# Kernel tuning notes

Measured on AMD Instinct MI355X. Metric: run time of the kernel, lower is better.

Reference implementation:

```python
import jax, jax.numpy as jnp
import numpy as np

B, D = 16384, 512


def setup_inputs() -> dict:
    key = jax.random.key(0)
    ks = jax.random.split(key, 7)
    s1 = 1.0 / np.sqrt(D + 1)
    s2 = 1.0 / np.sqrt(2 * D + 1)
    return {
        "t": jax.random.uniform(ks[0], (1,), dtype=jnp.float32),
        "z": jax.random.normal(ks[1], (B, D), dtype=jnp.float32),
        "logp_z": jnp.zeros((B, 1), dtype=jnp.float32),
        "W1": jax.random.normal(ks[2], (2 * D, D + 1), dtype=jnp.float32) * s1,
        "b1": jax.random.normal(ks[3], (2 * D,), dtype=jnp.float32) * s1,
        "W2": jax.random.normal(ks[4], (D, 2 * D + 1), dtype=jnp.float32) * s2,
        "b2": jax.random.normal(ks[5], (D,), dtype=jnp.float32) * s2,
    }


def reference(t, z, logp_z, W1, b1, W2, b2):
    # CNF dynamics: dz/dt = fc2(concat(relu(fc1(concat(z, t))), t))
    batch = z.shape[0]
    tt = jnp.full((batch, 1), t[0], dtype=z.dtype)
    x = jnp.concatenate([z, tt], axis=1)            # [B, D+1]
    h_pre = x @ W1.T + b1                           # [B, 2D]
    h = jax.nn.relu(h_pre)
    x2 = jnp.concatenate([h, tt], axis=1)           # [B, 2D+1]
    dz_dt = x2 @ W2.T + b2                          # [B, D]

    # Exact Jacobian trace of linear-relu-linear block (closed form of the
    # per-dim autograd loop in trace_df_dz):
    #   tr J = sum_h relu'(h_pre[:,h]) * (sum_i W2[i,h] * W1[h,i])
    W2h = W2[:, : 2 * D]                            # drop time column, [D, 2D]
    W1z = W1[:, :D]                                 # drop time column, [2D, D]
    c = jnp.sum(W2h.T * W1z, axis=1)                # [2D]
    mask = (h_pre > 0).astype(z.dtype)              # relu'
    trace = mask @ c                                # [B]
    dlogp_z_dt = -trace[:, None]                    # [B, 1]
    return dz_dt, dlogp_z_dt
```

## Files before the change

### kernel.cpp

```cpp
#include <hip/hip_runtime.h>
#include <stdint.h>

#define B_   16384
#define D_   512
#define N1_  1024
#define K1_  512
#define N2_  512
#define K2_  1024

#define DELTA     4e-3f
#define RCAP      16u
#define OCAP      64u

typedef _Float16 f16x8 __attribute__((ext_vector_type(8)));
typedef _Float16 f16x4 __attribute__((ext_vector_type(4)));
typedef float    f32x4 __attribute__((ext_vector_type(4)));

#define MFMA(a, b, c) __builtin_amdgcn_mfma_f32_16x16x32_f16(a, b, c, 0, 0, 0)

__global__ __launch_bounds__(256) void prep_w(
    const float* __restrict__ t,
    const float* __restrict__ W1, const float* __restrict__ b1,
    const float* __restrict__ W2, const float* __restrict__ b2,
    _Float16* __restrict__ wp,
    float* __restrict__ bias1, float* __restrict__ bias2,
    float* __restrict__ cvec) {
  int blk = blockIdx.x, tid = threadIdx.x;
  if (blk < 512) {
    int idx = blk * 256 + tid;
    int g = idx >> 11, rem = idx & 2047;
    int w = rem >> 8, nt = (rem >> 6) & 3, lane = rem & 63;
    int m16 = lane & 15, q = lane >> 4;
    int ch = g >> 5, ph = g & 31;
    const float* src;
    float scale;
    if (ph < 16) {
      int col = ch * 512 + w * 64 + nt * 16 + m16;
      int k = ph * 32 + q * 8;
      src = W1 + (size_t)col * 513 + k;
      scale = 64.f;
    } else {
      int col = w * 64 + nt * 16 + m16;
      int k = ch * 512 + (ph - 16) * 32 + q * 8;
      src = W2 + (size_t)col * 1025 + k;
      scale = 1.f;
    }
    f16x8 hv;
    #pragma unroll
    for (int e = 0; e < 8; ++e) hv[e] = (_Float16)(src[e] * scale);
    *(f16x8*)(wp + (size_t)idx * 8) = hv;
  } else if (blk < 516) {
    int j = (blk - 512) * 256 + tid;
    float t0 = t[0];
    bias1[j] = b1[j] + t0 * W1[(size_t)j * 513 + 512];
    if (j < 512) bias2[j] = b2[j] + t0 * W2[(size_t)j * 1025 + 1024];
  } else {
    int wave = tid >> 6, lane = tid & 63;
    int j = (blk - 516) * 4 + wave;
    float s = 0.f;
    #pragma unroll
    for (int kk = 0; kk < 8; ++kk) {
      int k = lane + kk * 64;
      s += W2[(size_t)k * 1025 + j] * W1[(size_t)j * 513 + k];
    }
    #pragma unroll
    for (int off = 32; off > 0; off >>= 1) s += __shfl_xor(s, off);
    if (lane == 0) cvec[j] = s;
  }
}


__global__ __launch_bounds__(512) void fused_kernel(
    const float* __restrict__ z, const _Float16* __restrict__ wp,
    const float* __restrict__ W1f,
    const float* __restrict__ bias1, const float* __restrict__ bias2,
    const float* __restrict__ cvec,
    float* __restrict__ out, float* __restrict__ dlogp) {
  __shared__ __align__(16) _Float16 Az[64 * 512];
  __shared__ __align__(16) _Float16 Hb[64 * 512];
  __shared__ __align__(16) float bias1L[1024];
  __shared__ __align__(16) float cvecL[1024];
  __shared__ uint32_t rbuck[64][RCAP];
  __shared__ uint32_t rbcnt[64];
  __shared__ uint32_t ovf[OCAP];
  __shared__ float redbuf[8][64];
  __shared__ float fixv[64];
  __shared__ float fixo[64];
  __shared__ uint32_t ovfcnt;

  const int tid  = threadIdx.x;
  const int lane = tid & 63, w = tid >> 6;
  const int q    = lane >> 4, m16 = lane & 15;
  const int sw   = m16 & 7;
  const int bm   = blockIdx.x;

  if (tid < 64) { rbcnt[tid] = 0; fixo[tid] = 0.f; }
  if (tid == 0) ovfcnt = 0;

  {
    const float* zp = z + (size_t)bm * 64 * 512;
    #pragma unroll
    for (int i = 0; i < 16; ++i) {
      int slot = i * 512 + tid;
      int row = slot >> 7, u8 = slot & 127;
      f32x4 v = *(const f32x4*)(zp + (size_t)row * 512 + u8 * 4);
      f16x4 hv;
      #pragma unroll
      for (int r = 0; r < 4; ++r) hv[r] = (_Float16)(v[r] * 16.f);
      int gz = (u8 >> 1) ^ (row & 7);
      *(f16x4*)((char*)Az + row * 1024 + gz * 16 + (u8 & 1) * 8) = hv;
    }
  }
  for (int i = tid; i < 1024; i += 512) {
    bias1L[i] = bias1[i];
    cvecL[i]  = cvec[i];
  }
  __syncthreads();

  f32x4 acc1[4][4] = {};
  f32x4 acc2[4][4] = {};
  float tr[4] = {0.f, 0.f, 0.f, 0.f};

  const char* azb   = (const char*)Az + m16 * 1024;
  const char* hbb   = (const char*)Hb + m16 * 1024;
  const char* wbase = (const char*)wp + w * 4096 + lane * 16;

  f16x8 cwA[4], cwB[4];
  #pragma unroll
  for (int nt = 0; nt < 4; ++nt) cwA[nt] = *(const f16x8*)(wbase + nt * 1024);

  for (int ch = 0; ch < 2; ++ch) {
    for (int s2 = 0; s2 < 8; ++s2) {
      const int s = s2 * 2;
      const int g = ch * 32 + s;
      #pragma unroll
      for (int nt = 0; nt < 4; ++nt)
        cwB[nt] = *(const f16x8*)(wbase + (size_t)(g + 1) * 32768 + nt * 1024);
      {
        const int zg = ((s * 4 + q) ^ sw) << 4;
        f16x8 zf0 = *(const f16x8*)(azb + 0 * 16384 + zg);
        f16x8 zf1 = *(const f16x8*)(azb + 1 * 16384 + zg);
        f16x8 zf2 = *(const f16x8*)(azb + 2 * 16384 + zg);
        f16x8 zf3 = *(const f16x8*)(azb + 3 * 16384 + zg);
        __builtin_amdgcn_s_setprio(1);
        #pragma unroll
        for (int nt = 0; nt < 4; ++nt) {
          acc1[0][nt] = MFMA(cwA[nt], zf0, acc1[0][nt]);
          acc1[1][nt] = MFMA(cwA[nt], zf1, acc1[1][nt]);
          acc1[2][nt] = MFMA(cwA[nt], zf2, acc1[2][nt]);
          acc1[3][nt] = MFMA(cwA[nt], zf3, acc1[3][nt]);
        }
        __builtin_amdgcn_s_setprio(0);
      }
      {
        const int gn = (g + 2 > 63) ? 63 : (g + 2);
        #pragma unroll
        for (int nt = 0; nt < 4; ++nt)
          cwA[nt] = *(const f16x8*)(wbase + (size_t)gn * 32768 + nt * 1024);
      }
      {
        const int zg = (((s + 1) * 4 + q) ^ sw) << 4;
        f16x8 zf0 = *(const f16x8*)(azb + 0 * 16384 + zg);
        f16x8 zf1 = *(const f16x8*)(azb + 1 * 16384 + zg);
        f16x8 zf2 = *(const f16x8*)(azb + 2 * 16384 + zg);
        f16x8 zf3 = *(const f16x8*)(azb + 3 * 16384 + zg);
        __builtin_amdgcn_s_setprio(1);
        #pragma unroll
        for (int nt = 0; nt < 4; ++nt) {
          acc1[0][nt] = MFMA(cwB[nt], zf0, acc1[0][nt]);
          acc1[1][nt] = MFMA(cwB[nt], zf1, acc1[1][nt]);
          acc1[2][nt] = MFMA(cwB[nt], zf2, acc1[2][nt]);
          acc1[3][nt] = MFMA(cwB[nt], zf3, acc1[3][nt]);
        }
        __builtin_amdgcn_s_setprio(0);
      }
    }

    __syncthreads();

    #pragma unroll
    for (int nt = 0; nt < 4; ++nt) {
      int colc = w * 64 + nt * 16 + q * 4;
      int col = ch * 512 + colc;
      f32x4 b4 = *(const f32x4*)&bias1L[col];
      f32x4 c4 = *(const f32x4*)&cvecL[col];
      #pragma unroll
      for (int mt = 0; mt < 4; ++mt) {
        int row = mt * 16 + m16;
        f16x4 hv;
        #pragma unroll
        for (int r = 0; r < 4; ++r) {
          float hp = acc1[mt][nt][r] * (1.f / 1024.f) + b4[r];
          hv[r] = (_Float16)(hp > 0.f ? hp : 0.f);
          if (hp > 0.f) tr[mt] += c4[r];
          if (__builtin_fabsf(hp) < DELTA) {
            uint32_t e = (uint32_t)(col + r) | (hp > 0.f ? 0x80000000u : 0u);
            uint32_t bi = atomicAdd(&rbcnt[row], 1u);
            if (bi < RCAP) rbuck[row][bi] = e;
            else {
              uint32_t oi = atomicAdd(&ovfcnt, 1u);
              if (oi < OCAP) ovf[oi] = ((uint32_t)row << 10) | e;
            }
          }
        }
        int gg = (colc >> 3) ^ (row & 7);
        *(f16x4*)((char*)Hb + row * 1024 + gg * 16 + (q & 1) * 8) = hv;
        acc1[mt][nt] = (f32x4){0.f, 0.f, 0.f, 0.f};
      }
    }

    __syncthreads();

    for (int t2 = 0; t2 < 8; ++t2) {
      const int t = t2 * 2;
      const int g = ch * 32 + 16 + t;
      #pragma unroll
      for (int nt = 0; nt < 4; ++nt)
        cwB[nt] = *(const f16x8*)(wbase + (size_t)(g + 1) * 32768 + nt * 1024);
      {
        const int hg = ((t * 4 + q) ^ sw) << 4;
        f16x8 hf0 = *(const f16x8*)(hbb + 0 * 16384 + hg);
        f16x8 hf1 = *(const f16x8*)(hbb + 1 * 16384 + hg);
        f16x8 hf2 = *(const f16x8*)(hbb + 2 * 16384 + hg);
        f16x8 hf3 = *(const f16x8*)(hbb + 3 * 16384 + hg);
        __builtin_amdgcn_s_setprio(1);
        #pragma unroll
        for (int nt = 0; nt < 4; ++nt) {
          acc2[0][nt] = MFMA(cwA[nt], hf0, acc2[0][nt]);
          acc2[1][nt] = MFMA(cwA[nt], hf1, acc2[1][nt]);
          acc2[2][nt] = MFMA(cwA[nt], hf2, acc2[2][nt]);
          acc2[3][nt] = MFMA(cwA[nt], hf3, acc2[3][nt]);
        }
        __builtin_amdgcn_s_setprio(0);
      }
      {
        const int gn = (g + 2 > 63) ? 63 : (g + 2);
        #pragma unroll
        for (int nt = 0; nt < 4; ++nt)
          cwA[nt] = *(const f16x8*)(wbase + (size_t)gn * 32768 + nt * 1024);
      }
      {
        const int hg = (((t + 1) * 4 + q) ^ sw) << 4;
        f16x8 hf0 = *(const f16x8*)(hbb + 0 * 16384 + hg);
        f16x8 hf1 = *(const f16x8*)(hbb + 1 * 16384 + hg);
        f16x8 hf2 = *(const f16x8*)(hbb + 2 * 16384 + hg);
        f16x8 hf3 = *(const f16x8*)(hbb + 3 * 16384 + hg);
        __builtin_amdgcn_s_setprio(1);
        #pragma unroll
        for (int nt = 0; nt < 4; ++nt) {
          acc2[0][nt] = MFMA(cwB[nt], hf0, acc2[0][nt]);
          acc2[1][nt] = MFMA(cwB[nt], hf1, acc2[1][nt]);
          acc2[2][nt] = MFMA(cwB[nt], hf2, acc2[2][nt]);
          acc2[3][nt] = MFMA(cwB[nt], hf3, acc2[3][nt]);
        }
        __builtin_amdgcn_s_setprio(0);
      }
    }
  }

  #pragma unroll
  for (int mt = 0; mt < 4; ++mt) {
    int row = bm * 64 + mt * 16 + m16;
    #pragma unroll
    for (int nt = 0; nt < 4; ++nt) {
      int col = w * 64 + nt * 16 + q * 4;
      f32x4 b2v = *(const f32x4*)(bias2 + col);
      *(f32x4*)(out + (size_t)row * 512 + col) = acc2[mt][nt] + b2v;
    }
  }

  #pragma unroll
  for (int mt = 0; mt < 4; ++mt) {
    tr[mt] += __shfl_xor(tr[mt], 16);
    tr[mt] += __shfl_xor(tr[mt], 32);
  }
  if (q == 0) {
    #pragma unroll
    for (int mt = 0; mt < 4; ++mt) redbuf[w][mt * 16 + m16] = tr[mt];
  }
  __syncthreads();

  #pragma unroll 1
  for (int r8 = 0; r8 < 8; ++r8) {
    int row = w * 8 + r8;
    uint32_t cnt = rbcnt[row];
    if (cnt > RCAP) cnt = RCAP;
    float corr = 0.f;
    if (cnt) {
      const float* zr = z + ((size_t)(bm * 64 + row)) * 512;
      float zv[8];
      #pragma unroll
      for (int it = 0; it < 8; ++it) zv[it] = zr[it * 64 + lane];
      for (uint32_t e = 0; e < cnt; ++e) {
        uint32_t en = rbuck[row][e];
        int col  = (int)(en & 1023u);
        int oldm = (int)(en >> 31);
        const float* wc = W1f + (size_t)col * 513;
        float s = 0.f;
        #pragma unroll
        for (int it = 0; it < 8; ++it) s += zv[it] * wc[it * 64 + lane];
        #pragma unroll
        for (int off = 32; off > 0; off >>= 1) s += __shfl_xor(s, off);
        float hp = s + bias1L[col];
        int newm = hp > 0.f ? 1 : 0;
        if (newm != oldm) corr += oldm ? cvecL[col] : -cvecL[col];
      }
    }
    if (lane == 0) fixv[row] = corr;
  }
  {
    uint32_t on = ovfcnt;
    if (on > OCAP) on = OCAP;
    for (uint32_t i = w; i < on; i += 8) {
      uint32_t e = ovf[i];
      int row  = (int)((e >> 10) & 63u);
      int col  = (int)(e & 1023u);
      int oldm = (int)(e >> 31);
      const float* zr = z + ((size_t)(bm * 64 + row)) * 512;
      const float* wc = W1f + (size_t)col * 513;
      float s = 0.f;
      #pragma unroll
      for (int it = 0; it < 8; ++it) {
        int k = it * 64 + lane;
        s += zr[k] * wc[k];
      }
      #pragma unroll
      for (int off = 32; off > 0; off >>= 1) s += __shfl_xor(s, off);
      if (lane == 0) {
        float hp = s + bias1L[col];
        int newm = hp > 0.f ? 1 : 0;
        if (newm != oldm) atomicAdd(&fixo[row], oldm ? cvecL[col] : -cvecL[col]);
      }
    }
  }
  __syncthreads();

  if (tid < 64) {
    float s = 0.f;
    #pragma unroll
    for (int ww = 0; ww < 8; ++ww) s += redbuf[ww][tid];
    dlogp[bm * 64 + tid] = -s + fixv[tid] + fixo[tid];
  }
}

extern "C" void kernel_launch(void* const* d_in, const int* in_sizes, int n_in,
                              void* d_out, int out_size, void* d_ws, size_t ws_size,
                              hipStream_t stream) {
  const float* t  = (const float*)d_in[0];
  const float* z  = (const float*)d_in[1];
  const float* W1 = (const float*)d_in[3];
  const float* b1 = (const float*)d_in[4];
  const float* W2 = (const float*)d_in[5];
  const float* b2 = (const float*)d_in[6];

  float* out   = (float*)d_out;
  float* dlogp = out + (size_t)B_ * D_;

  char* ws = (char*)d_ws;
  _Float16* wp    = (_Float16*)ws; ws += (size_t)64 * 32768;
  float*    bias1 = (float*)ws;    ws += 1024 * 4;
  float*    bias2 = (float*)ws;    ws += 512 * 4;
  float*    cvec  = (float*)ws;    ws += 1024 * 4;

  prep_w<<<772, 256, 0, stream>>>(t, W1, b1, W2, b2, wp, bias1, bias2, cvec);
  fused_kernel<<<256, 512, 0, stream>>>(z, wp, W1, bias1, bias2, cvec, out, dlogp);
}
```

Baseline: 157.5 us.

## Halve row tile to 32 and drop weight double-buffering for higher occupancy

Each block now processes 32 rows instead of 64, doubling the grid to 512 blocks and halving the shared-memory and accumulator footprint. The explicit register double-buffering of weight fragments is replaced with a simpler unrolled loop, and launch bounds request more resident waves. This targets latency hiding through occupancy, but weights are reloaded twice as often per row, so L2 traffic roughly doubles. The tighter register bound may also cause spills.

```diff
diff --git a/kernel.cpp b/kernel.cpp
--- a/kernel.cpp
+++ b/kernel.cpp
@@ -10,7 +10,7 @@
 
 #define DELTA     4e-3f
 #define RCAP      16u
-#define OCAP      64u
+#define OCAP      32u
 
 typedef _Float16 f16x8 __attribute__((ext_vector_type(8)));
 typedef _Float16 f16x4 __attribute__((ext_vector_type(4)));
@@ -70,22 +70,22 @@
 }
 
 
-__global__ __launch_bounds__(512) void fused_kernel(
+__global__ __launch_bounds__(512, 4) void fused_kernel(
     const float* __restrict__ z, const _Float16* __restrict__ wp,
     const float* __restrict__ W1f,
     const float* __restrict__ bias1, const float* __restrict__ bias2,
     const float* __restrict__ cvec,
     float* __restrict__ out, float* __restrict__ dlogp) {
-  __shared__ __align__(16) _Float16 Az[64 * 512];
-  __shared__ __align__(16) _Float16 Hb[64 * 512];
+  __shared__ __align__(16) _Float16 Az[32 * 512];
+  __shared__ __align__(16) _Float16 Hb[32 * 512];
   __shared__ __align__(16) float bias1L[1024];
   __shared__ __align__(16) float cvecL[1024];
-  __shared__ uint32_t rbuck[64][RCAP];
-  __shared__ uint32_t rbcnt[64];
+  __shared__ uint32_t rbuck[32][RCAP];
+  __shared__ uint32_t rbcnt[32];
   __shared__ uint32_t ovf[OCAP];
-  __shared__ float redbuf[8][64];
-  __shared__ float fixv[64];
-  __shared__ float fixo[64];
+  __shared__ float redbuf[8][32];
+  __shared__ float fixv[32];
+  __shared__ float fixo[32];
   __shared__ uint32_t ovfcnt;
 
   const int tid  = threadIdx.x;
@@ -94,13 +94,13 @@
   const int sw   = m16 & 7;
   const int bm   = blockIdx.x;
 
-  if (tid < 64) { rbcnt[tid] = 0; fixo[tid] = 0.f; }
+  if (tid < 32) { rbcnt[tid] = 0; fixo[tid] = 0.f; }
   if (tid == 0) ovfcnt = 0;
 
   {
-    const float* zp = z + (size_t)bm * 64 * 512;
-    #pragma unroll
-    for (int i = 0; i < 16; ++i) {
+    const float* zp = z + (size_t)bm * 32 * 512;
+    #pragma unroll
+    for (int i = 0; i < 8; ++i) {
       int slot = i * 512 + tid;
       int row = slot >> 7, u8 = slot & 127;
       f32x4 v = *(const f32x4*)(zp + (size_t)row * 512 + u8 * 4);
@@ -117,63 +117,35 @@
   }
   __syncthreads();
 
-  f32x4 acc1[4][4] = {};
-  f32x4 acc2[4][4] = {};
-  float tr[4] = {0.f, 0.f, 0.f, 0.f};
+  f32x4 acc1[2][4] = {};
+  f32x4 acc2[2][4] = {};
+  float tr[2] = {0.f, 0.f};
 
   const char* azb   = (const char*)Az + m16 * 1024;
   const char* hbb   = (const char*)Hb + m16 * 1024;
   const char* wbase = (const char*)wp + w * 4096 + lane * 16;
 
-  f16x8 cwA[4], cwB[4];
-  #pragma unroll
-  for (int nt = 0; nt < 4; ++nt) cwA[nt] = *(const f16x8*)(wbase + nt * 1024);
-
   for (int ch = 0; ch < 2; ++ch) {
-    for (int s2 = 0; s2 < 8; ++s2) {
-      const int s = s2 * 2;
-      const int g = ch * 32 + s;
-      #pragma unroll
-      for (int nt = 0; nt < 4; ++nt)
-        cwB[nt] = *(const f16x8*)(wbase + (size_t)(g + 1) * 32768 + nt * 1024);
-      {
-        const int zg = ((s * 4 + q) ^ sw) << 4;
-        f16x8 zf0 = *(const f16x8*)(azb + 0 * 16384 + zg);
-        f16x8 zf1 = *(const f16x8*)(azb + 1 * 16384 + zg);
-        f16x8 zf2 = *(const f16x8*)(azb + 2 * 16384 + zg);
-        f16x8 zf3 = *(const f16x8*)(azb + 3 * 16384 + zg);
-        __builtin_amdgcn_s_setprio(1);
-        #pragma unroll
-        for (int nt = 0; nt < 4; ++nt) {
-          acc1[0][nt] = MFMA(cwA[nt], zf0, acc1[0][nt]);
-          acc1[1][nt] = MFMA(cwA[nt], zf1, acc1[1][nt]);
-          acc1[2][nt] = MFMA(cwA[nt], zf2, acc1[2][nt]);
-          acc1[3][nt] = MFMA(cwA[nt], zf3, acc1[3][nt]);
-        }
-        __builtin_amdgcn_s_setprio(0);
-      }
-      {
-        const int gn = (g + 2 > 63) ? 63 : (g + 2);
-        #pragma unroll
-        for (int nt = 0; nt < 4; ++nt)
-          cwA[nt] = *(const f16x8*)(wbase + (size_t)gn * 32768 + nt * 1024);
-      }
-      {
-        const int zg = (((s + 1) * 4 + q) ^ sw) << 4;
-        f16x8 zf0 = *(const f16x8*)(azb + 0 * 16384 + zg);
-        f16x8 zf1 = *(const f16x8*)(azb + 1 * 16384 + zg);
-        f16x8 zf2 = *(const f16x8*)(azb + 2 * 16384 + zg);
-        f16x8 zf3 = *(const f16x8*)(azb + 3 * 16384 + zg);
-        __builtin_amdgcn_s_setprio(1);
-        #pragma unroll
-        for (int nt = 0; nt < 4; ++nt) {
-          acc1[0][nt] = MFMA(cwB[nt], zf0, acc1[0][nt]);
-          acc1[1][nt] = MFMA(cwB[nt], zf1, acc1[1][nt]);
-          acc1[2][nt] = MFMA(cwB[nt], zf2, acc1[2][nt]);
-          acc1[3][nt] = MFMA(cwB[nt], zf3, acc1[3][nt]);
-        }
-        __builtin_amdgcn_s_setprio(0);
-      }
+    #pragma unroll 4
+    for (int s = 0; s < 16; ++s) {
+      const char* wsl = wbase + (size_t)(ch * 32 + s) * 32768;
+      f16x8 cw0 = *(const f16x8*)(wsl);
+      f16x8 cw1 = *(const f16x8*)(wsl + 1024);
+      f16x8 cw2 = *(const f16x8*)(wsl + 2048);
+      f16x8 cw3 = *(const f16x8*)(wsl + 3072);
+      const int zg = ((s * 4 + q) ^ sw) << 4;
+      f16x8 zf0 = *(const f16x8*)(azb + zg);
+      f16x8 zf1 = *(const f16x8*)(azb + 16384 + zg);
+      __builtin_amdgcn_s_setprio(1);
+      acc1[0][0] = MFMA(cw0, zf0, acc1[0][0]);
+      acc1[0][1] = MFMA(cw1, zf0, acc1[0][1]);
+      acc1[0][2] = MFMA(cw2, zf0, acc1[0][2]);
+      acc1[0][3] = MFMA(cw3, zf0, acc1[0][3]);
+      acc1[1][0] = MFMA(cw0, zf1, acc1[1][0]);
+      acc1[1][1] = MFMA(cw1, zf1, acc1[1][1]);
+      acc1[1][2] = MFMA(cw2, zf1, acc1[1][2]);
+      acc1[1][3] = MFMA(cw3, zf1, acc1[1][3]);
+      __builtin_amdgcn_s_setprio(0);
     }
 
     __syncthreads();
@@ -185,7 +157,7 @@
       f32x4 b4 = *(const f32x4*)&bias1L[col];
       f32x4 c4 = *(const f32x4*)&cvecL[col];
       #pragma unroll
-      for (int mt = 0; mt < 4; ++mt) {
+      for (int mt = 0; mt < 2; ++mt) {
         int row = mt * 16 + m16;
         f16x4 hv;
         #pragma unroll
@@ -211,56 +183,32 @@
 
     __syncthreads();
 
-    for (int t2 = 0; t2 < 8; ++t2) {
-      const int t = t2 * 2;
-      const int g = ch * 32 + 16 + t;
-      #pragma unroll
-      for (int nt = 0; nt < 4; ++nt)
-        cwB[nt] = *(const f16x8*)(wbase + (size_t)(g + 1) * 32768 + nt * 1024);
-      {
-        const int hg = ((t * 4 + q) ^ sw) << 4;
-        f16x8 hf0 = *(const f16x8*)(hbb + 0 * 16384 + hg);
-        f16x8 hf1 = *(const f16x8*)(hbb + 1 * 16384 + hg);
-        f16x8 hf2 = *(const f16x8*)(hbb + 2 * 16384 + hg);
-        f16x8 hf3 = *(const f16x8*)(hbb + 3 * 16384 + hg);
-        __builtin_amdgcn_s_setprio(1);
-        #pragma unroll
-        for (int nt = 0; nt < 4; ++nt) {
-          acc2[0][nt] = MFMA(cwA[nt], hf0, acc2[0][nt]);
-          acc2[1][nt] = MFMA(cwA[nt], hf1, acc2[1][nt]);
-          acc2[2][nt] = MFMA(cwA[nt], hf2, acc2[2][nt]);
-          acc2[3][nt] = MFMA(cwA[nt], hf3, acc2[3][nt]);
-        }
-        __builtin_amdgcn_s_setprio(0);
-      }
-      {
-        const int gn = (g + 2 > 63) ? 63 : (g + 2);
-        #pragma unroll
-        for (int nt = 0; nt < 4; ++nt)
-          cwA[nt] = *(const f16x8*)(wbase + (size_t)gn * 32768 + nt * 1024);
-      }
-      {
-        const int hg = (((t + 1) * 4 + q) ^ sw) << 4;
-        f16x8 hf0 = *(const f16x8*)(hbb + 0 * 16384 + hg);
-        f16x8 hf1 = *(const f16x8*)(hbb + 1 * 16384 + hg);
-        f16x8 hf2 = *(const f16x8*)(hbb + 2 * 16384 + hg);
-        f16x8 hf3 = *(const f16x8*)(hbb + 3 * 16384 + hg);
-        __builtin_amdgcn_s_setprio(1);
-        #pragma unroll
-        for (int nt = 0; nt < 4; ++nt) {
-          acc2[0][nt] = MFMA(cwB[nt], hf0, acc2[0][nt]);
-          acc2[1][nt] = MFMA(cwB[nt], hf1, acc2[1][nt]);
-          acc2[2][nt] = MFMA(cwB[nt], hf2, acc2[2][nt]);
-          acc2[3][nt] = MFMA(cwB[nt], hf3, acc2[3][nt]);
-        }
-        __builtin_amdgcn_s_setprio(0);
-      }
+    #pragma unroll 4
+    for (int t = 0; t < 16; ++t) {
+      const char* wsl = wbase + (size_t)(ch * 32 + 16 + t) * 32768;
+      f16x8 cw0 = *(const f16x8*)(wsl);
+      f16x8 cw1 = *(const f16x8*)(wsl + 1024);
+      f16x8 cw2 = *(const f16x8*)(wsl + 2048);
+      f16x8 cw3 = *(const f16x8*)(wsl + 3072);
+      const int hg = ((t * 4 + q) ^ sw) << 4;
+      f16x8 hf0 = *(const f16x8*)(hbb + hg);
+      f16x8 hf1 = *(const f16x8*)(hbb + 16384 + hg);
+      __builtin_amdgcn_s_setprio(1);
+      acc2[0][0] = MFMA(cw0, hf0, acc2[0][0]);
+      acc2[0][1] = MFMA(cw1, hf0, acc2[0][1]);
+      acc2[0][2] = MFMA(cw2, hf0, acc2[0][2]);
+      acc2[0][3] = MFMA(cw3, hf0, acc2[0][3]);
+      acc2[1][0] = MFMA(cw0, hf1, acc2[1][0]);
+      acc2[1][1] = MFMA(cw1, hf1, acc2[1][1]);
+      acc2[1][2] = MFMA(cw2, hf1, acc2[1][2]);
+      acc2[1][3] = MFMA(cw3, hf1, acc2[1][3]);
+      __builtin_amdgcn_s_setprio(0);
     }
   }
 
   #pragma unroll
-  for (int mt = 0; mt < 4; ++mt) {
-    int row = bm * 64 + mt * 16 + m16;
+  for (int mt = 0; mt < 2; ++mt) {
+    int row = bm * 32 + mt * 16 + m16;
     #pragma unroll
     for (int nt = 0; nt < 4; ++nt) {
       int col = w * 64 + nt * 16 + q * 4;
@@ -270,24 +218,24 @@
   }
 
   #pragma unroll
-  for (int mt = 0; mt < 4; ++mt) {
+  for (int mt = 0; mt < 2; ++mt) {
     tr[mt] += __shfl_xor(tr[mt], 16);
     tr[mt] += __shfl_xor(tr[mt], 32);
   }
   if (q == 0) {
     #pragma unroll
-    for (int mt = 0; mt < 4; ++mt) redbuf[w][mt * 16 + m16] = tr[mt];
+    for (int mt = 0; mt < 2; ++mt) redbuf[w][mt * 16 + m16] = tr[mt];
   }
   __syncthreads();
 
   #pragma unroll 1
-  for (int r8 = 0; r8 < 8; ++r8) {
-    int row = w * 8 + r8;
+  for (int r4 = 0; r4 < 4; ++r4) {
+    int row = w * 4 + r4;
     uint32_t cnt = rbcnt[row];
     if (cnt > RCAP) cnt = RCAP;
     float corr = 0.f;
     if (cnt) {
-      const float* zr = z + ((size_t)(bm * 64 + row)) * 512;
+      const float* zr = z + ((size_t)(bm * 32 + row)) * 512;
       float zv[8];
       #pragma unroll
       for (int it = 0; it < 8; ++it) zv[it] = zr[it * 64 + lane];
@@ -313,10 +261,10 @@
     if (on > OCAP) on = OCAP;
     for (uint32_t i = w; i < on; i += 8) {
       uint32_t e = ovf[i];
-      int row  = (int)((e >> 10) & 63u);
+      int row  = (int)((e >> 10) & 31u);
       int col  = (int)(e & 1023u);
       int oldm = (int)(e >> 31);
-      const float* zr = z + ((size_t)(bm * 64 + row)) * 512;
+      const float* zr = z + ((size_t)(bm * 32 + row)) * 512;
       const float* wc = W1f + (size_t)col * 513;
       float s = 0.f;
       #pragma unroll
@@ -335,11 +283,11 @@
   }
   __syncthreads();
 
-  if (tid < 64) {
+  if (tid < 32) {
     float s = 0.f;
     #pragma unroll
     for (int ww = 0; ww < 8; ++ww) s += redbuf[ww][tid];
-    dlogp[bm * 64 + tid] = -s + fixv[tid] + fixo[tid];
+    dlogp[bm * 32 + tid] = -s + fixv[tid] + fixo[tid];
   }
 }
 
@@ -363,5 +311,5 @@
   float*    cvec  = (float*)ws;    ws += 1024 * 4;
 
   prep_w<<<772, 256, 0, stream>>>(t, W1, b1, W2, b2, wp, bias1, bias2, cvec);
-  fused_kernel<<<256, 512, 0, stream>>>(z, wp, W1, bias1, bias2, cvec, out, dlogp);
+  fused_kernel<<<512, 512, 0, stream>>>(z, wp, W1, bias1, bias2, cvec, out, dlogp);
 }
```

Result: slower. 162.9 us (+3.4%).

## Double waves per block to 16 with half-width N tiles and prefetch W1 rows in fixup

Applied to the files above, without the earlier changes.

Raises the fused kernel block from 512 to 1024 threads. Each of the 16 waves now owns 32 output columns instead of 64, which halves per-wave accumulator and weight-register state and doubles the waves available to hide MFMA and load latency. The near-threshold fixup loop also prefetches the next W1 row while reducing the current one, and the overflow capacity is reduced. The cost is that each loaded z/h fragment feeds fewer MFMAs, LDS fragment traffic per FLOP rises, and register pressure is constrained by the 1024-thread launch bound.

```diff
diff --git a/kernel.cpp b/kernel.cpp
--- a/kernel.cpp
+++ b/kernel.cpp
@@ -10,7 +10,7 @@
 
 #define DELTA     4e-3f
 #define RCAP      16u
-#define OCAP      64u
+#define OCAP      32u
 
 typedef _Float16 f16x8 __attribute__((ext_vector_type(8)));
 typedef _Float16 f16x4 __attribute__((ext_vector_type(4)));
@@ -70,7 +70,7 @@
 }
 
 
-__global__ __launch_bounds__(512) void fused_kernel(
+__global__ __launch_bounds__(1024, 4) void fused_kernel(
     const float* __restrict__ z, const _Float16* __restrict__ wp,
     const float* __restrict__ W1f,
     const float* __restrict__ bias1, const float* __restrict__ bias2,
@@ -83,7 +83,7 @@
   __shared__ uint32_t rbuck[64][RCAP];
   __shared__ uint32_t rbcnt[64];
   __shared__ uint32_t ovf[OCAP];
-  __shared__ float redbuf[8][64];
+  __shared__ float redbuf[16][64];
   __shared__ float fixv[64];
   __shared__ float fixo[64];
   __shared__ uint32_t ovfcnt;
@@ -100,8 +100,8 @@
   {
     const float* zp = z + (size_t)bm * 64 * 512;
     #pragma unroll
-    for (int i = 0; i < 16; ++i) {
-      int slot = i * 512 + tid;
+    for (int i = 0; i < 8; ++i) {
+      int slot = i * 1024 + tid;
       int row = slot >> 7, u8 = slot & 127;
       f32x4 v = *(const f32x4*)(zp + (size_t)row * 512 + u8 * 4);
       f16x4 hv;
@@ -111,67 +111,67 @@
       *(f16x4*)((char*)Az + row * 1024 + gz * 16 + (u8 & 1) * 8) = hv;
     }
   }
-  for (int i = tid; i < 1024; i += 512) {
-    bias1L[i] = bias1[i];
-    cvecL[i]  = cvec[i];
+  if (tid < 1024) {
+    bias1L[tid] = bias1[tid];
+    cvecL[tid]  = cvec[tid];
   }
   __syncthreads();
 
-  f32x4 acc1[4][4] = {};
-  f32x4 acc2[4][4] = {};
+  f32x4 acc1[4][2] = {};
+  f32x4 acc2[4][2] = {};
   float tr[4] = {0.f, 0.f, 0.f, 0.f};
 
   const char* azb   = (const char*)Az + m16 * 1024;
   const char* hbb   = (const char*)Hb + m16 * 1024;
-  const char* wbase = (const char*)wp + w * 4096 + lane * 16;
-
-  f16x8 cwA[4], cwB[4];
-  #pragma unroll
-  for (int nt = 0; nt < 4; ++nt) cwA[nt] = *(const f16x8*)(wbase + nt * 1024);
+  const char* wbase = (const char*)wp + (w >> 1) * 4096 + (w & 1) * 2048 + lane * 16;
+
+  f16x8 cwA[2], cwB[2];
+  cwA[0] = *(const f16x8*)(wbase);
+  cwA[1] = *(const f16x8*)(wbase + 1024);
 
   for (int ch = 0; ch < 2; ++ch) {
     for (int s2 = 0; s2 < 8; ++s2) {
       const int s = s2 * 2;
       const int g = ch * 32 + s;
-      #pragma unroll
-      for (int nt = 0; nt < 4; ++nt)
-        cwB[nt] = *(const f16x8*)(wbase + (size_t)(g + 1) * 32768 + nt * 1024);
+      cwB[0] = *(const f16x8*)(wbase + (size_t)(g + 1) * 32768);
+      cwB[1] = *(const f16x8*)(wbase + (size_t)(g + 1) * 32768 + 1024);
       {
         const int zg = ((s * 4 + q) ^ sw) << 4;
-        f16x8 zf0 = *(const f16x8*)(azb + 0 * 16384 + zg);
-        f16x8 zf1 = *(const f16x8*)(azb + 1 * 16384 + zg);
-        f16x8 zf2 = *(const f16x8*)(azb + 2 * 16384 + zg);
-        f16x8 zf3 = *(const f16x8*)(azb + 3 * 16384 + zg);
+        f16x8 zf0 = *(const f16x8*)(azb + zg);
+        f16x8 zf1 = *(const f16x8*)(azb + 16384 + zg);
+        f16x8 zf2 = *(const f16x8*)(azb + 32768 + zg);
+        f16x8 zf3 = *(const f16x8*)(azb + 49152 + zg);
         __builtin_amdgcn_s_setprio(1);
-        #pragma unroll
-        for (int nt = 0; nt < 4; ++nt) {
-          acc1[0][nt] = MFMA(cwA[nt], zf0, acc1[0][nt]);
-          acc1[1][nt] = MFMA(cwA[nt], zf1, acc1[1][nt]);
-          acc1[2][nt] = MFMA(cwA[nt], zf2, acc1[2][nt]);
-          acc1[3][nt] = MFMA(cwA[nt], zf3, acc1[3][nt]);
-        }
+        acc1[0][0] = MFMA(cwA[0], zf0, acc1[0][0]);
+        acc1[0][1] = MFMA(cwA[1], zf0, acc1[0][1]);
+        acc1[1][0] = MFMA(cwA[0], zf1, acc1[1][0]);
+        acc1[1][1] = MFMA(cwA[1], zf1, acc1[1][1]);
+        acc1[2][0] = MFMA(cwA[0], zf2, acc1[2][0]);
+        acc1[2][1] = MFMA(cwA[1], zf2, acc1[2][1]);
+        acc1[3][0] = MFMA(cwA[0], zf3, acc1[3][0]);
+        acc1[3][1] = MFMA(cwA[1], zf3, acc1[3][1]);
         __builtin_amdgcn_s_setprio(0);
       }
       {
         const int gn = (g + 2 > 63) ? 63 : (g + 2);
-        #pragma unroll
-        for (int nt = 0; nt < 4; ++nt)
-          cwA[nt] = *(const f16x8*)(wbase + (size_t)gn * 32768 + nt * 1024);
+        cwA[0] = *(const f16x8*)(wbase + (size_t)gn * 32768);
+        cwA[1] = *(const f16x8*)(wbase + (size_t)gn * 32768 + 1024);
       }
       {
         const int zg = (((s + 1) * 4 + q) ^ sw) << 4;
-        f16x8 zf0 = *(const f16x8*)(azb + 0 * 16384 + zg);
-        f16x8 zf1 = *(const f16x8*)(azb + 1 * 16384 + zg);
-        f16x8 zf2 = *(const f16x8*)(azb + 2 * 16384 + zg);
-        f16x8 zf3 = *(const f16x8*)(azb + 3 * 16384 + zg);
+        f16x8 zf0 = *(const f16x8*)(azb + zg);
+        f16x8 zf1 = *(const f16x8*)(azb + 16384 + zg);
+        f16x8 zf2 = *(const f16x8*)(azb + 32768 + zg);
+        f16x8 zf3 = *(const f16x8*)(azb + 49152 + zg);
         __builtin_amdgcn_s_setprio(1);
-        #pragma unroll
-        for (int nt = 0; nt < 4; ++nt) {
-          acc1[0][nt] = MFMA(cwB[nt], zf0, acc1[0][nt]);
-          acc1[1][nt] = MFMA(cwB[nt], zf1, acc1[1][nt]);
-          acc1[2][nt] = MFMA(cwB[nt], zf2, acc1[2][nt]);
-          acc1[3][nt] = MFMA(cwB[nt], zf3, acc1[3][nt]);
-        }
+        acc1[0][0] = MFMA(cwB[0], zf0, acc1[0][0]);
+        acc1[0][1] = MFMA(cwB[1], zf0, acc1[0][1]);
+        acc1[1][0] = MFMA(cwB[0], zf1, acc1[1][0]);
+        acc1[1][1] = MFMA(cwB[1], zf1, acc1[1][1]);
+        acc1[2][0] = MFMA(cwB[0], zf2, acc1[2][0]);
+        acc1[2][1] = MFMA(cwB[1], zf2, acc1[2][1]);
+        acc1[3][0] = MFMA(cwB[0], zf3, acc1[3][0]);
+        acc1[3][1] = MFMA(cwB[1], zf3, acc1[3][1]);
         __builtin_amdgcn_s_setprio(0);
       }
     }
@@ -179,8 +179,8 @@
     __syncthreads();
 
     #pragma unroll
-    for (int nt = 0; nt < 4; ++nt) {
-      int colc = w * 64 + nt * 16 + q * 4;
+    for (int nt = 0; nt < 2; ++nt) {
+      int colc = w * 32 + nt * 16 + q * 4;
       int col = ch * 512 + colc;
       f32x4 b4 = *(const f32x4*)&bias1L[col];
       f32x4 c4 = *(const f32x4*)&cvecL[col];
@@ -214,45 +214,45 @@
     for (int t2 = 0; t2 < 8; ++t2) {
       const int t = t2 * 2;
       const int g = ch * 32 + 16 + t;
-      #pragma unroll
-      for (int nt = 0; nt < 4; ++nt)
-        cwB[nt] = *(const f16x8*)(wbase + (size_t)(g + 1) * 32768 + nt * 1024);
+      cwB[0] = *(const f16x8*)(wbase + (size_t)(g + 1) * 32768);
+      cwB[1] = *(const f16x8*)(wbase + (size_t)(g + 1) * 32768 + 1024);
       {
         const int hg = ((t * 4 + q) ^ sw) << 4;
-        f16x8 hf0 = *(const f16x8*)(hbb + 0 * 16384 + hg);
-        f16x8 hf1 = *(const f16x8*)(hbb + 1 * 16384 + hg);
-        f16x8 hf2 = *(const f16x8*)(hbb + 2 * 16384 + hg);
-        f16x8 hf3 = *(const f16x8*)(hbb + 3 * 16384 + hg);
+        f16x8 hf0 = *(const f16x8*)(hbb + hg);
+        f16x8 hf1 = *(const f16x8*)(hbb + 16384 + hg);
+        f16x8 hf2 = *(const f16x8*)(hbb + 32768 + hg);
+        f16x8 hf3 = *(const f16x8*)(hbb + 49152 + hg);
         __builtin_amdgcn_s_setprio(1);
-        #pragma unroll
-        for (int nt = 0; nt < 4; ++nt) {
-          acc2[0][nt] = MFMA(cwA[nt], hf0, acc2[0][nt]);
-          acc2[1][nt] = MFMA(cwA[nt], hf1, acc2[1][nt]);
-          acc2[2][nt] = MFMA(cwA[nt], hf2, acc2[2][nt]);
-          acc2[3][nt] = MFMA(cwA[nt], hf3, acc2[3][nt]);
-        }
+        acc2[0][0] = MFMA(cwA[0], hf0, acc2[0][0]);
+        acc2[0][1] = MFMA(cwA[1], hf0, acc2[0][1]);
+        acc2[1][0] = MFMA(cwA[0], hf1, acc2[1][0]);
+        acc2[1][1] = MFMA(cwA[1], hf1, acc2[1][1]);
+        acc2[2][0] = MFMA(cwA[0], hf2, acc2[2][0]);
+        acc2[2][1] = MFMA(cwA[1], hf2, acc2[2][1]);
+        acc2[3][0] = MFMA(cwA[0], hf3, acc2[3][0]);
+        acc2[3][1] = MFMA(cwA[1], hf3, acc2[3][1]);
         __builtin_amdgcn_s_setprio(0);
       }
       {
         const int gn = (g + 2 > 63) ? 63 : (g + 2);
-        #pragma unroll
-        for (int nt = 0; nt < 4; ++nt)
-          cwA[nt] = *(const f16x8*)(wbase + (size_t)gn * 32768 + nt * 1024);
+        cwA[0] = *(const f16x8*)(wbase + (size_t)gn * 32768);
+        cwA[1] = *(const f16x8*)(wbase + (size_t)gn * 32768 + 1024);
       }
       {
         const int hg = (((t + 1) * 4 + q) ^ sw) << 4;
-        f16x8 hf0 = *(const f16x8*)(hbb + 0 * 16384 + hg);
-        f16x8 hf1 = *(const f16x8*)(hbb + 1 * 16384 + hg);
-        f16x8 hf2 = *(const f16x8*)(hbb + 2 * 16384 + hg);
-        f16x8 hf3 = *(const f16x8*)(hbb + 3 * 16384 + hg);
+        f16x8 hf0 = *(const f16x8*)(hbb + hg);
+        f16x8 hf1 = *(const f16x8*)(hbb + 16384 + hg);
+        f16x8 hf2 = *(const f16x8*)(hbb + 32768 + hg);
+        f16x8 hf3 = *(const f16x8*)(hbb + 49152 + hg);
         __builtin_amdgcn_s_setprio(1);
-        #pragma unroll
-        for (int nt = 0; nt < 4; ++nt) {
-          acc2[0][nt] = MFMA(cwB[nt], hf0, acc2[0][nt]);
-          acc2[1][nt] = MFMA(cwB[nt], hf1, acc2[1][nt]);
-          acc2[2][nt] = MFMA(cwB[nt], hf2, acc2[2][nt]);
-          acc2[3][nt] = MFMA(cwB[nt], hf3, acc2[3][nt]);
-        }
+        acc2[0][0] = MFMA(cwB[0], hf0, acc2[0][0]);
+        acc2[0][1] = MFMA(cwB[1], hf0, acc2[0][1]);
+        acc2[1][0] = MFMA(cwB[0], hf1, acc2[1][0]);
+        acc2[1][1] = MFMA(cwB[1], hf1, acc2[1][1]);
+        acc2[2][0] = MFMA(cwB[0], hf2, acc2[2][0]);
+        acc2[2][1] = MFMA(cwB[1], hf2, acc2[2][1]);
+        acc2[3][0] = MFMA(cwB[0], hf3, acc2[3][0]);
+        acc2[3][1] = MFMA(cwB[1], hf3, acc2[3][1]);
         __builtin_amdgcn_s_setprio(0);
       }
     }
@@ -262,8 +262,8 @@
   for (int mt = 0; mt < 4; ++mt) {
     int row = bm * 64 + mt * 16 + m16;
     #pragma unroll
-    for (int nt = 0; nt < 4; ++nt) {
-      int col = w * 64 + nt * 16 + q * 4;
+    for (int nt = 0; nt < 2; ++nt) {
+      int col = w * 32 + nt * 16 + q * 4;
       f32x4 b2v = *(const f32x4*)(bias2 + col);
       *(f32x4*)(out + (size_t)row * 512 + col) = acc2[mt][nt] + b2v;
     }
@@ -281,8 +281,8 @@
   __syncthreads();
 
   #pragma unroll 1
-  for (int r8 = 0; r8 < 8; ++r8) {
-    int row = w * 8 + r8;
+  for (int r4 = 0; r4 < 4; ++r4) {
+    int row = w * 4 + r4;
     uint32_t cnt = rbcnt[row];
     if (cnt > RCAP) cnt = RCAP;
     float corr = 0.f;
@@ -291,19 +291,31 @@
       float zv[8];
       #pragma unroll
       for (int it = 0; it < 8; ++it) zv[it] = zr[it * 64 + lane];
+      uint32_t en = rbuck[row][0];
+      const float* wc0 = W1f + (size_t)(en & 1023u) * 513;
+      float wv[8];
+      #pragma unroll
+      for (int it = 0; it < 8; ++it) wv[it] = wc0[it * 64 + lane];
       for (uint32_t e = 0; e < cnt; ++e) {
-        uint32_t en = rbuck[row][e];
         int col  = (int)(en & 1023u);
         int oldm = (int)(en >> 31);
-        const float* wc = W1f + (size_t)col * 513;
+        float wn[8];
+        if (e + 1 < cnt) {
+          en = rbuck[row][e + 1];
+          const float* wcn = W1f + (size_t)(en & 1023u) * 513;
+          #pragma unroll
+          for (int it = 0; it < 8; ++it) wn[it] = wcn[it * 64 + lane];
+        }
         float s = 0.f;
         #pragma unroll
-        for (int it = 0; it < 8; ++it) s += zv[it] * wc[it * 64 + lane];
+        for (int it = 0; it < 8; ++it) s += zv[it] * wv[it];
         #pragma unroll
         for (int off = 32; off > 0; off >>= 1) s += __shfl_xor(s, off);
         float hp = s + bias1L[col];
         int newm = hp > 0.f ? 1 : 0;
         if (newm != oldm) corr += oldm ? cvecL[col] : -cvecL[col];
+        #pragma unroll
+        for (int it = 0; it < 8; ++it) wv[it] = wn[it];
       }
     }
     if (lane == 0) fixv[row] = corr;
@@ -311,7 +323,7 @@
   {
     uint32_t on = ovfcnt;
     if (on > OCAP) on = OCAP;
-    for (uint32_t i = w; i < on; i += 8) {
+    for (uint32_t i = w; i < on; i += 16) {
       uint32_t e = ovf[i];
       int row  = (int)((e >> 10) & 63u);
       int col  = (int)(e & 1023u);
@@ -338,7 +350,7 @@
   if (tid < 64) {
     float s = 0.f;
     #pragma unroll
-    for (int ww = 0; ww < 8; ++ww) s += redbuf[ww][tid];
+    for (int ww = 0; ww < 16; ++ww) s += redbuf[ww][tid];
     dlogp[bm * 64 + tid] = -s + fixv[tid] + fixo[tid];
   }
 }
@@ -363,5 +375,5 @@
   float*    cvec  = (float*)ws;    ws += 1024 * 4;
 
   prep_w<<<772, 256, 0, stream>>>(t, W1, b1, W2, b2, wp, bias1, bias2, cvec);
-  fused_kernel<<<256, 512, 0, stream>>>(z, wp, W1, bias1, bias2, cvec, out, dlogp);
+  fused_kernel<<<256, 1024, 0, stream>>>(z, wp, W1, bias1, bias2, cvec, out, dlogp);
 }
```

New measurement: 159.6 us. No clear change (+1.3%).

## Software-pipeline LDS fragment loads in GEMM loops and pair correction entries per wave

Applied to the files above, without the earlier changes.

The MFMA main loops now load only two of the four activation row-fragments ahead and overlap the other two loads with the MFMAs of the current half, a register-level double buffer across row tiles that trims live registers and hides LDS latency. The near-zero pre-activation correction pass now lets each half-wave handle a different bucket entry, so two fp32 recomputations run at once per wave. The overflow capacity is halved. This adds scheduling complexity and a risk of dropping corrections if overflow exceeds the smaller cap.

```diff
diff --git a/kernel.cpp b/kernel.cpp
--- a/kernel.cpp
+++ b/kernel.cpp
@@ -10,7 +10,7 @@
 
 #define DELTA     4e-3f
 #define RCAP      16u
-#define OCAP      64u
+#define OCAP      32u
 
 typedef _Float16 f16x8 __attribute__((ext_vector_type(8)));
 typedef _Float16 f16x4 __attribute__((ext_vector_type(4)));
@@ -126,52 +126,98 @@
   const char* wbase = (const char*)wp + w * 4096 + lane * 16;
 
   f16x8 cwA[4], cwB[4];
-  #pragma unroll
-  for (int nt = 0; nt < 4; ++nt) cwA[nt] = *(const f16x8*)(wbase + nt * 1024);
+  f16x8 zc0, zc1, zn0, zn1;
+  {
+    const char* wb = wbase;
+    cwA[0] = *(const f16x8*)(wb);
+    cwA[1] = *(const f16x8*)(wb + 1024);
+    cwA[2] = *(const f16x8*)(wb + 2048);
+    cwA[3] = *(const f16x8*)(wb + 3072);
+  }
 
   for (int ch = 0; ch < 2; ++ch) {
+    {
+      const int zg = (q ^ sw) << 4;
+      zc0 = *(const f16x8*)(azb + zg);
+      zc1 = *(const f16x8*)(azb + 16384 + zg);
+    }
     for (int s2 = 0; s2 < 8; ++s2) {
       const int s = s2 * 2;
       const int g = ch * 32 + s;
-      #pragma unroll
-      for (int nt = 0; nt < 4; ++nt)
-        cwB[nt] = *(const f16x8*)(wbase + (size_t)(g + 1) * 32768 + nt * 1024);
+      {
+        const char* wb = wbase + (size_t)(g + 1) * 32768;
+        cwB[0] = *(const f16x8*)(wb);
+        cwB[1] = *(const f16x8*)(wb + 1024);
+        cwB[2] = *(const f16x8*)(wb + 2048);
+        cwB[3] = *(const f16x8*)(wb + 3072);
+      }
       {
         const int zg = ((s * 4 + q) ^ sw) << 4;
-        f16x8 zf0 = *(const f16x8*)(azb + 0 * 16384 + zg);
-        f16x8 zf1 = *(const f16x8*)(azb + 1 * 16384 + zg);
-        f16x8 zf2 = *(const f16x8*)(azb + 2 * 16384 + zg);
-        f16x8 zf3 = *(const f16x8*)(azb + 3 * 16384 + zg);
-        __builtin_amdgcn_s_setprio(1);
-        #pragma unroll
-        for (int nt = 0; nt < 4; ++nt) {
-          acc1[0][nt] = MFMA(cwA[nt], zf0, acc1[0][nt]);
-          acc1[1][nt] = MFMA(cwA[nt], zf1, acc1[1][nt]);
-          acc1[2][nt] = MFMA(cwA[nt], zf2, acc1[2][nt]);
-          acc1[3][nt] = MFMA(cwA[nt], zf3, acc1[3][nt]);
-        }
+        zn0 = *(const f16x8*)(azb + 32768 + zg);
+        zn1 = *(const f16x8*)(azb + 49152 + zg);
+        __builtin_amdgcn_s_setprio(1);
+        acc1[0][0] = MFMA(cwA[0], zc0, acc1[0][0]);
+        acc1[0][1] = MFMA(cwA[1], zc0, acc1[0][1]);
+        acc1[0][2] = MFMA(cwA[2], zc0, acc1[0][2]);
+        acc1[0][3] = MFMA(cwA[3], zc0, acc1[0][3]);
+        acc1[1][0] = MFMA(cwA[0], zc1, acc1[1][0]);
+        acc1[1][1] = MFMA(cwA[1], zc1, acc1[1][1]);
+        acc1[1][2] = MFMA(cwA[2], zc1, acc1[1][2]);
+        acc1[1][3] = MFMA(cwA[3], zc1, acc1[1][3]);
+        __builtin_amdgcn_s_setprio(0);
+      }
+      {
+        const int zg = (((s + 1) * 4 + q) ^ sw) << 4;
+        zc0 = *(const f16x8*)(azb + zg);
+        zc1 = *(const f16x8*)(azb + 16384 + zg);
+        __builtin_amdgcn_s_setprio(1);
+        acc1[2][0] = MFMA(cwA[0], zn0, acc1[2][0]);
+        acc1[2][1] = MFMA(cwA[1], zn0, acc1[2][1]);
+        acc1[2][2] = MFMA(cwA[2], zn0, acc1[2][2]);
+        acc1[2][3] = MFMA(cwA[3], zn0, acc1[2][3]);
+        acc1[3][0] = MFMA(cwA[0], zn1, acc1[3][0]);
+        acc1[3][1] = MFMA(cwA[1], zn1, acc1[3][1]);
+        acc1[3][2] = MFMA(cwA[2], zn1, acc1[3][2]);
+        acc1[3][3] = MFMA(cwA[3], zn1, acc1[3][3]);
         __builtin_amdgcn_s_setprio(0);
       }
       {
         const int gn = (g + 2 > 63) ? 63 : (g + 2);
-        #pragma unroll
-        for (int nt = 0; nt < 4; ++nt)
-          cwA[nt] = *(const f16x8*)(wbase + (size_t)gn * 32768 + nt * 1024);
+        const char* wb = wbase + (size_t)gn * 32768;
+        cwA[0] = *(const f16x8*)(wb);
+        cwA[1] = *(const f16x8*)(wb + 1024);
+        cwA[2] = *(const f16x8*)(wb + 2048);
+        cwA[3] = *(const f16x8*)(wb + 3072);
       }
       {
         const int zg = (((s + 1) * 4 + q) ^ sw) << 4;
-        f16x8 zf0 = *(const f16x8*)(azb + 0 * 16384 + zg);
-        f16x8 zf1 = *(const f16x8*)(azb + 1 * 16384 + zg);
-        f16x8 zf2 = *(const f16x8*)(azb + 2 * 16384 + zg);
-        f16x8 zf3 = *(const f16x8*)(azb + 3 * 16384 + zg);
-        __builtin_amdgcn_s_setprio(1);
-        #pragma unroll
-        for (int nt = 0; nt < 4; ++nt) {
-          acc1[0][nt] = MFMA(cwB[nt], zf0, acc1[0][nt]);
-          acc1[1][nt] = MFMA(cwB[nt], zf1, acc1[1][nt]);
-          acc1[2][nt] = MFMA(cwB[nt], zf2, acc1[2][nt]);
-          acc1[3][nt] = MFMA(cwB[nt], zf3, acc1[3][nt]);
-        }
+        zn0 = *(const f16x8*)(azb + 32768 + zg);
+        zn1 = *(const f16x8*)(azb + 49152 + zg);
+        __builtin_amdgcn_s_setprio(1);
+        acc1[0][0] = MFMA(cwB[0], zc0, acc1[0][0]);
+        acc1[0][1] = MFMA(cwB[1], zc0, acc1[0][1]);
+        acc1[0][2] = MFMA(cwB[2], zc0, acc1[0][2]);
+        acc1[0][3] = MFMA(cwB[3], zc0, acc1[0][3]);
+        acc1[1][0] = MFMA(cwB[0], zc1, acc1[1][0]);
+        acc1[1][1] = MFMA(cwB[1], zc1, acc1[1][1]);
+        acc1[1][2] = MFMA(cwB[2], zc1, acc1[1][2]);
+        acc1[1][3] = MFMA(cwB[3], zc1, acc1[1][3]);
+        __builtin_amdgcn_s_setprio(0);
+      }
+      {
+        const int sn = (s + 2 > 15) ? 15 : (s + 2);
+        const int zg = ((sn * 4 + q) ^ sw) << 4;
+        zc0 = *(const f16x8*)(azb + zg);
+        zc1 = *(const f16x8*)(azb + 16384 + zg);
+        __builtin_amdgcn_s_setprio(1);
+        acc1[2][0] = MFMA(cwB[0], zn0, acc1[2][0]);
+        acc1[2][1] = MFMA(cwB[1], zn0, acc1[2][1]);
+        acc1[2][2] = MFMA(cwB[2], zn0, acc1[2][2]);
+        acc1[2][3] = MFMA(cwB[3], zn0, acc1[2][3]);
+        acc1[3][0] = MFMA(cwB[0], zn1, acc1[3][0]);
+        acc1[3][1] = MFMA(cwB[1], zn1, acc1[3][1]);
+        acc1[3][2] = MFMA(cwB[2], zn1, acc1[3][2]);
+        acc1[3][3] = MFMA(cwB[3], zn1, acc1[3][3]);
         __builtin_amdgcn_s_setprio(0);
       }
     }
@@ -211,48 +257,88 @@
 
     __syncthreads();
 
+    {
+      const int zg = (q ^ sw) << 4;
+      zc0 = *(const f16x8*)(hbb + zg);
+      zc1 = *(const f16x8*)(hbb + 16384 + zg);
+    }
     for (int t2 = 0; t2 < 8; ++t2) {
       const int t = t2 * 2;
       const int g = ch * 32 + 16 + t;
-      #pragma unroll
-      for (int nt = 0; nt < 4; ++nt)
-        cwB[nt] = *(const f16x8*)(wbase + (size_t)(g + 1) * 32768 + nt * 1024);
-      {
-        const int hg = ((t * 4 + q) ^ sw) << 4;
-        f16x8 hf0 = *(const f16x8*)(hbb + 0 * 16384 + hg);
-        f16x8 hf1 = *(const f16x8*)(hbb + 1 * 16384 + hg);
-        f16x8 hf2 = *(const f16x8*)(hbb + 2 * 16384 + hg);
-        f16x8 hf3 = *(const f16x8*)(hbb + 3 * 16384 + hg);
-        __builtin_amdgcn_s_setprio(1);
-        #pragma unroll
-        for (int nt = 0; nt < 4; ++nt) {
-          acc2[0][nt] = MFMA(cwA[nt], hf0, acc2[0][nt]);
-          acc2[1][nt] = MFMA(cwA[nt], hf1, acc2[1][nt]);
-          acc2[2][nt] = MFMA(cwA[nt], hf2, acc2[2][nt]);
-          acc2[3][nt] = MFMA(cwA[nt], hf3, acc2[3][nt]);
-        }
+      {
+        const char* wb = wbase + (size_t)(g + 1) * 32768;
+        cwB[0] = *(const f16x8*)(wb);
+        cwB[1] = *(const f16x8*)(wb + 1024);
+        cwB[2] = *(const f16x8*)(wb + 2048);
+        cwB[3] = *(const f16x8*)(wb + 3072);
+      }
+      {
+        const int zg = ((t * 4 + q) ^ sw) << 4;
+        zn0 = *(const f16x8*)(hbb + 32768 + zg);
+        zn1 = *(const f16x8*)(hbb + 49152 + zg);
+        __builtin_amdgcn_s_setprio(1);
+        acc2[0][0] = MFMA(cwA[0], zc0, acc2[0][0]);
+        acc2[0][1] = MFMA(cwA[1], zc0, acc2[0][1]);
+        acc2[0][2] = MFMA(cwA[2], zc0, acc2[0][2]);
+        acc2[0][3] = MFMA(cwA[3], zc0, acc2[0][3]);
+        acc2[1][0] = MFMA(cwA[0], zc1, acc2[1][0]);
+        acc2[1][1] = MFMA(cwA[1], zc1, acc2[1][1]);
+        acc2[1][2] = MFMA(cwA[2], zc1, acc2[1][2]);
+        acc2[1][3] = MFMA(cwA[3], zc1, acc2[1][3]);
+        __builtin_amdgcn_s_setprio(0);
+      }
+      {
+        const int zg = (((t + 1) * 4 + q) ^ sw) << 4;
+        zc0 = *(const f16x8*)(hbb + zg);
+        zc1 = *(const f16x8*)(hbb + 16384 + zg);
+        __builtin_amdgcn_s_setprio(1);
+        acc2[2][0] = MFMA(cwA[0], zn0, acc2[2][0]);
+        acc2[2][1] = MFMA(cwA[1], zn0, acc2[2][1]);
+        acc2[2][2] = MFMA(cwA[2], zn0, acc2[2][2]);
+        acc2[2][3] = MFMA(cwA[3], zn0, acc2[2][3]);
+        acc2[3][0] = MFMA(cwA[0], zn1, acc2[3][0]);
+        acc2[3][1] = MFMA(cwA[1], zn1, acc2[3][1]);
+        acc2[3][2] = MFMA(cwA[2], zn1, acc2[3][2]);
+        acc2[3][3] = MFMA(cwA[3], zn1, acc2[3][3]);
         __builtin_amdgcn_s_setprio(0);
       }
       {
         const int gn = (g + 2 > 63) ? 63 : (g + 2);
-        #pragma unroll
-        for (int nt = 0; nt < 4; ++nt)
-          cwA[nt] = *(const f16x8*)(wbase + (size_t)gn * 32768 + nt * 1024);
-      }
-      {
-        const int hg = (((t + 1) * 4 + q) ^ sw) << 4;
-        f16x8 hf0 = *(const f16x8*)(hbb + 0 * 16384 + hg);
-        f16x8 hf1 = *(const f16x8*)(hbb + 1 * 16384 + hg);
-        f16x8 hf2 = *(const f16x8*)(hbb + 2 * 16384 + hg);
-        f16x8 hf3 = *(const f16x8*)(hbb + 3 * 16384 + hg);
-        __builtin_amdgcn_s_setprio(1);
-        #pragma unroll
-        for (int nt = 0; nt < 4; ++nt) {
-          acc2[0][nt] = MFMA(cwB[nt], hf0, acc2[0][nt]);
-          acc2[1][nt] = MFMA(cwB[nt], hf1, acc2[1][nt]);
-          acc2[2][nt] = MFMA(cwB[nt], hf2, acc2[2][nt]);
-          acc2[3][nt] = MFMA(cwB[nt], hf3, acc2[3][nt]);
-        }
+        const char* wb = wbase + (size_t)gn * 32768;
+        cwA[0] = *(const f16x8*)(wb);
+        cwA[1] = *(const f16x8*)(wb + 1024);
+        cwA[2] = *(const f16x8*)(wb + 2048);
+        cwA[3] = *(const f16x8*)(wb + 3072);
+      }
+      {
+        const int zg = (((t + 1) * 4 + q) ^ sw) << 4;
+        zn0 = *(const f16x8*)(hbb + 32768 + zg);
+        zn1 = *(const f16x8*)(hbb + 49152 + zg);
+        __builtin_amdgcn_s_setprio(1);
+        acc2[0][0] = MFMA(cwB[0], zc0, acc2[0][0]);
+        acc2[0][1] = MFMA(cwB[1], zc0, acc2[0][1]);
+        acc2[0][2] = MFMA(cwB[2], zc0, acc2[0][2]);
+        acc2[0][3] = MFMA(cwB[3], zc0, acc2[0][3]);
+        acc2[1][0] = MFMA(cwB[0], zc1, acc2[1][0]);
+        acc2[1][1] = MFMA(cwB[1], zc1, acc2[1][1]);
+        acc2[1][2] = MFMA(cwB[2], zc1, acc2[1][2]);
+        acc2[1][3] = MFMA(cwB[3], zc1, acc2[1][3]);
+        __builtin_amdgcn_s_setprio(0);
+      }
+      {
+        const int tn = (t + 2 > 15) ? 15 : (t + 2);
+        const int zg = ((tn * 4 + q) ^ sw) << 4;
+        zc0 = *(const f16x8*)(hbb + zg);
+        zc1 = *(const f16x8*)(hbb + 16384 + zg);
+        __builtin_amdgcn_s_setprio(1);
+        acc2[2][0] = MFMA(cwB[0], zn0, acc2[2][0]);
+        acc2[2][1] = MFMA(cwB[1], zn0, acc2[2][1]);
+        acc2[2][2] = MFMA(cwB[2], zn0, acc2[2][2]);
+        acc2[2][3] = MFMA(cwB[3], zn0, acc2[2][3]);
+        acc2[3][0] = MFMA(cwB[0], zn1, acc2[3][0]);
+        acc2[3][1] = MFMA(cwB[1], zn1, acc2[3][1]);
+        acc2[3][2] = MFMA(cwB[2], zn1, acc2[3][2]);
+        acc2[3][3] = MFMA(cwB[3], zn1, acc2[3][3]);
         __builtin_amdgcn_s_setprio(0);
       }
     }
@@ -280,33 +366,41 @@
   }
   __syncthreads();
 
-  #pragma unroll 1
-  for (int r8 = 0; r8 < 8; ++r8) {
-    int row = w * 8 + r8;
-    uint32_t cnt = rbcnt[row];
-    if (cnt > RCAP) cnt = RCAP;
-    float corr = 0.f;
-    if (cnt) {
-      const float* zr = z + ((size_t)(bm * 64 + row)) * 512;
-      float zv[8];
-      #pragma unroll
-      for (int it = 0; it < 8; ++it) zv[it] = zr[it * 64 + lane];
-      for (uint32_t e = 0; e < cnt; ++e) {
-        uint32_t en = rbuck[row][e];
-        int col  = (int)(en & 1023u);
-        int oldm = (int)(en >> 31);
-        const float* wc = W1f + (size_t)col * 513;
-        float s = 0.f;
+  {
+    const int hlane = lane & 31;
+    const int half  = lane >> 5;
+    #pragma unroll 1
+    for (int r8 = 0; r8 < 8; ++r8) {
+      int row = w * 8 + r8;
+      uint32_t cnt = rbcnt[row];
+      if (cnt > RCAP) cnt = RCAP;
+      float corr = 0.f;
+      if (cnt) {
+        const float* zr = z + ((size_t)(bm * 64 + row)) * 512;
+        float zv[16];
         #pragma unroll
-        for (int it = 0; it < 8; ++it) s += zv[it] * wc[it * 64 + lane];
-        #pragma unroll
-        for (int off = 32; off > 0; off >>= 1) s += __shfl_xor(s, off);
-        float hp = s + bias1L[col];
-        int newm = hp > 0.f ? 1 : 0;
-        if (newm != oldm) corr += oldm ? cvecL[col] : -cvecL[col];
-      }
-    }
-    if (lane == 0) fixv[row] = corr;
+        for (int it = 0; it < 16; ++it) zv[it] = zr[it * 32 + hlane];
+        for (uint32_t e = 0; e < cnt; e += 2) {
+          uint32_t idx = e + (uint32_t)half;
+          int act = idx < cnt;
+          uint32_t en = rbuck[row][act ? idx : e];
+          int col  = (int)(en & 1023u);
+          int oldm = (int)(en >> 31);
+          const float* wc = W1f + (size_t)col * 513;
+          float s = 0.f;
+          #pragma unroll
+          for (int it = 0; it < 16; ++it) s += zv[it] * wc[it * 32 + hlane];
+          #pragma unroll
+          for (int off = 16; off > 0; off >>= 1) s += __shfl_xor(s, off);
+          float hp = s + bias1L[col];
+          int newm = hp > 0.f ? 1 : 0;
+          float delta = (act && newm != oldm) ? (oldm ? cvecL[col] : -cvecL[col]) : 0.f;
+          delta += __shfl_xor(delta, 32);
+          corr += delta;
+        }
+      }
+      if (lane == 0) fixv[row] = corr;
+    }
   }
   {
     uint32_t on = ovfcnt;
```

Measured after the change: 150.6 us. -4.4%, faster.
